# Optimization experiments

Hardware: AMD Instinct MI355X
Metric: run time of the kernel (lower is better)

Reference implementation:

```python
import jax, jax.numpy as jnp
import numpy as np
import math

B, T, D, H = 2, 2048, 1024, 16
HD = D // H  # head_dim = 64
ROPE_BASE = 10000.0


def _rope_tables(t_len, dim, base, dtype=jnp.float32):
    inv_freq = 1.0 / (base ** (jnp.arange(0, dim, 2, dtype=jnp.float32) / dim))
    t = jnp.arange(t_len, dtype=jnp.float32)
    freqs = jnp.outer(t, inv_freq)                 # [T, dim/2]
    emb = jnp.concatenate([freqs, freqs], axis=-1)  # [T, dim]
    return jnp.cos(emb).astype(dtype), jnp.sin(emb).astype(dtype)


def _rotate_half(x):
    x1, x2 = jnp.split(x, 2, axis=-1)
    return jnp.concatenate([-x2, x1], axis=-1)


def _apply_rotary(x, cos, sin):
    # x: [B,H,T,hd]; cos/sin: [T,hd] broadcast over B,H
    return x * cos[None, None, :, :] + _rotate_half(x) * sin[None, None, :, :]


def setup_inputs() -> dict:
    key = jax.random.key(0)
    ks = jax.random.split(key, 5)
    x = jax.random.normal(ks[0], (B, T, D), dtype=jnp.float32)
    Wq = jax.random.normal(ks[1], (D, D), dtype=jnp.float32) * (1.0 / math.sqrt(D))
    Wk = jax.random.normal(ks[2], (D, D), dtype=jnp.float32) * (1.0 / math.sqrt(D))
    Wv = jax.random.normal(ks[3], (D, D), dtype=jnp.float32) * (1.0 / math.sqrt(D))
    Wo = jax.random.normal(ks[4], (D, D), dtype=jnp.float32) * (1.0 / math.sqrt(D))
    # additive causal mask: 0 on/below diagonal, -inf above
    neg = jnp.finfo(jnp.float32).min
    mask = jnp.where(jnp.tril(jnp.ones((T, T), dtype=bool)), 0.0, neg).astype(jnp.float32)
    return {"x": x, "mask": mask, "Wq": Wq, "Wk": Wk, "Wv": Wv, "Wo": Wo}


def reference(x, mask, Wq, Wk, Wv, Wo):
    scale = math.sqrt(HD)
    # projections (nn.Linear: y = x @ W.T), split heads -> [B,H,T,hd]
    q = jnp.einsum('btd,ed->bte', x, Wq).reshape(B, T, H, HD).transpose(0, 2, 1, 3)
    k = jnp.einsum('btd,ed->bte', x, Wk).reshape(B, T, H, HD).transpose(0, 2, 1, 3)
    v = jnp.einsum('btd,ed->bte', x, Wv).reshape(B, T, H, HD).transpose(0, 2, 1, 3)
    cos, sin = _rope_tables(T, HD, ROPE_BASE, x.dtype)
    q = _apply_rotary(q, cos, sin)
    k = _apply_rotary(k, cos, sin)
    scores = jnp.einsum('bhqd,bhkd->bhqk', q, k) / scale   # [B,H,T,T]
    scores = scores + mask[None, None, :, :]
    attn_weights = jax.nn.softmax(scores, axis=-1)          # [B,H,T,T]
    # dropout=0.0 (eval): attn_weights_dropped == attn_weights
    out = jnp.einsum('bhqk,bhkd->bhqd', attn_weights, v)    # [B,H,T,hd]
    out = out.transpose(0, 2, 1, 3).reshape(B, T, D)
    out = jnp.einsum('btd,ed->bte', out, Wo)
    return out, attn_weights
```

## Files before the change

### kernel.cpp

```cpp
#include <hip/hip_runtime.h>
#include <math.h>

#define Tn 2048
#define Dn 1024
#define Hn 16
#define HDn 64

typedef float f32x4 __attribute__((ext_vector_type(4)));
typedef _Float16 f16x8 __attribute__((ext_vector_type(8)));
typedef _Float16 f16x4 __attribute__((ext_vector_type(4)));
typedef __fp16 fp16x2 __attribute__((ext_vector_type(2)));

__device__ __forceinline__ f32x4 mfma16(f16x8 a, f16x8 b, f32x4 c) {
  return __builtin_amdgcn_mfma_f32_16x16x32_f16(a, b, c, 0, 0, 0);
}

__device__ __forceinline__ void cvt_store4(_Float16* dst, float4 v) {
  union { _Float16 h[4]; uint2 u; } pk;
  pk.h[0] = (_Float16)v.x; pk.h[1] = (_Float16)v.y;
  pk.h[2] = (_Float16)v.z; pk.h[3] = (_Float16)v.w;
  *reinterpret_cast<uint2*>(dst) = pk.u;
}

__device__ __forceinline__ void nt_store4v(float* p, f32x4 t) {
  __builtin_nontemporal_store(t, reinterpret_cast<f32x4*>(p));
}

__device__ __forceinline__ f16x4 pk4(float a, float b, float c, float d) {
  union { fp16x2 v[2]; f16x4 h; } u;
  u.v[0] = __builtin_amdgcn_cvt_pkrtz(a, b);
  u.v[1] = __builtin_amdgcn_cvt_pkrtz(c, d);
  return u.h;
}

__device__ __forceinline__ void gld16(const _Float16* g, _Float16* l) {
  __builtin_amdgcn_global_load_lds(
      (const __attribute__((address_space(1))) uint32_t*)g,
      (__attribute__((address_space(3))) uint32_t*)l, 16, 0, 0);
}

#define SOFT_SYNC do {                                        \
    __builtin_amdgcn_sched_barrier(0);                        \
    asm volatile("s_waitcnt lgkmcnt(0)" ::: "memory");        \
    __builtin_amdgcn_s_barrier();                             \
    __builtin_amdgcn_sched_barrier(0);                        \
  } while (0)

__global__ __launch_bounds__(256) void cvt_fp16_kernel(
    const float* __restrict__ x, const float* __restrict__ wq,
    const float* __restrict__ wk, const float* __restrict__ wv,
    const float* __restrict__ wo,
    _Float16* __restrict__ xh, _Float16* __restrict__ wqh,
    _Float16* __restrict__ wkh, _Float16* __restrict__ wvh,
    _Float16* __restrict__ woh)
{
  int i = blockIdx.x * 256 + threadIdx.x;
  const float* src; _Float16* dst; int off;
  if (i < 1048576) { src = x; dst = xh; off = i; }
  else {
    int j = i - 1048576;
    int w = j >> 18; off = j & 262143;
    src = (w == 0) ? wq : (w == 1) ? wk : (w == 2) ? wv : wo;
    dst = (w == 0) ? wqh : (w == 1) ? wkh : (w == 2) ? wvh : woh;
  }
  float4 v = reinterpret_cast<const float4*>(src)[off];
  cvt_store4(dst + (size_t)off * 4, v);
}

__global__ void rope_table_kernel(float* __restrict__ cosT, float* __restrict__ sinT) {
  int i = blockIdx.x * 256 + threadIdx.x;
  if (i >= Tn * 32) return;
  int t = i >> 5, f = i & 31;
  float inv = powf(10000.0f, -(float)(2 * f) / 64.0f);
  float ang = (float)t * inv;
  float c = cosf(ang), s = sinf(ang);
  cosT[t * HDn + f] = c; cosT[t * HDn + f + 32] = c;
  sinT[t * HDn + f] = s; sinT[t * HDn + f + 32] = s;
}

__global__ __launch_bounds__(256) void proj_kernel(
    const _Float16* __restrict__ xh, const _Float16* __restrict__ wqh,
    const _Float16* __restrict__ wkh, const _Float16* __restrict__ wvh,
    const float* __restrict__ cosT, const float* __restrict__ sinT,
    _Float16* __restrict__ qh, _Float16* __restrict__ kh, _Float16* __restrict__ vh)
{
  const int w = blockIdx.z;
  const _Float16* __restrict__ W = (w == 0) ? wqh : (w == 1) ? wkh : wvh;
  _Float16* __restrict__ dst = (w == 0) ? qh : (w == 1) ? kh : vh;
  __shared__ alignas(16) _Float16 As[128 * 64];
  __shared__ alignas(16) _Float16 Bs[128 * 64];
  const int tid = threadIdx.x;
  const int lane = tid & 63, wave = tid >> 6;
  const int lrow = lane & 15, lhi = lane >> 4;
  const int wm = wave >> 1, wn = wave & 1;
  const int f = blockIdx.x, s = f >> 3;
  const int mt = (f & 7) + 8 * (s & 3);
  const int ntl = s >> 2;
  const int m0 = mt * 128, n0 = ntl * 128;
  f32x4 acc[4][4];
#pragma unroll
  for (int i = 0; i < 4; ++i)
#pragma unroll
    for (int j = 0; j < 4; ++j) acc[i][j] = f32x4{0.f, 0.f, 0.f, 0.f};

  for (int k0 = 0; k0 < Dn; k0 += 64) {
#pragma unroll
    for (int it = 0; it < 4; ++it) {
      int n = it * 256 + tid;
      int row = n >> 3, cc = n & 7;
      int csw = cc ^ (row & 7);
      _Float16* lbase = As + (size_t)(it * 256 + wave * 64) * 8;
      gld16(xh + (size_t)(m0 + row) * Dn + k0 + csw * 8, lbase);
      _Float16* lbase2 = Bs + (size_t)(it * 256 + wave * 64) * 8;
      gld16(W + (size_t)(n0 + row) * Dn + k0 + csw * 8, lbase2);
    }
    __syncthreads();
#pragma unroll
    for (int kc = 0; kc < 2; ++kc) {
      f16x8 af[4], bf[4];
#pragma unroll
      for (int i = 0; i < 4; ++i) {
        int row = wm * 64 + i * 16 + lrow;
        af[i] = *reinterpret_cast<const f16x8*>(
            As + row * 64 + (((kc * 4 + lhi) ^ (row & 7)) << 3));
      }
#pragma unroll
      for (int j = 0; j < 4; ++j) {
        int row = wn * 64 + j * 16 + lrow;
        bf[j] = *reinterpret_cast<const f16x8*>(
            Bs + row * 64 + (((kc * 4 + lhi) ^ (row & 7)) << 3));
      }
#pragma unroll
      for (int i = 0; i < 4; ++i)
#pragma unroll
        for (int j = 0; j < 4; ++j)
          acc[i][j] = mfma16(af[i], bf[j], acc[i][j]);
    }
    __syncthreads();
  }
  const bool isqk = (w < 2);
#pragma unroll
  for (int i = 0; i < 4; ++i) {
#pragma unroll
    for (int r = 0; r < 4; ++r) {
      int rowg = m0 + wm * 64 + i * 16 + lhi * 4 + r;
      int bb = rowg >> 11, t = rowg & (Tn - 1);
#pragma unroll
      for (int j = 0; j < 4; ++j) {
        int colg = n0 + wn * 64 + j * 16 + lrow;
        int hh = colg >> 6, d = colg & 63;
        float val = acc[i][j][r];
        if (isqk) {
          float partner = acc[i][j ^ 2][r];
          float rot = (j < 2) ? -partner : partner;
          val = val * cosT[t * HDn + d] + rot * sinT[t * HDn + d];
        }
        dst[(((size_t)(bb * Hn + hh)) * Tn + t) * HDn + d] = (_Float16)val;
      }
    }
  }
}

__global__ __launch_bounds__(256) void attn_kernel(
    const _Float16* __restrict__ qh, const _Float16* __restrict__ kh,
    const _Float16* __restrict__ vh, float* __restrict__ attnw,
    _Float16* __restrict__ obuf)
{
  const int f = blockIdx.x;
  const int s = f >> 3, g = s >> 5;
  const int my_bh = (f & 7) + 8 * g;
  const int c = ((s & 31) + 8 * g) & 31;
  const int b = my_bh >> 4, h = my_bh & 15;
  const size_t bh = (size_t)my_bh;
  const _Float16* __restrict__ Qp = qh + bh * Tn * HDn;
  const _Float16* __restrict__ Kp = kh + bh * Tn * HDn;
  const _Float16* __restrict__ Vp = vh + bh * Tn * HDn;
  float* __restrict__ attnp = attnw + bh * (size_t)Tn * Tn;

  __shared__ _Float16 Ks[128][72];
  __shared__ _Float16 Vt[64][136];
  __shared__ _Float16 Pt[4][16][136];

  const int tid = threadIdx.x;
  const int lane = tid & 63, wave = tid >> 6;
  const int q16 = lane & 15, lhi = lane >> 4;
  const int qp0 = c * 64;
  const int wrow = qp0 + wave * 16;
  const int qg = wrow + q16;
  const int ntiles = (c >> 1) + 1;

  f16x8 bq[2];
#pragma unroll
  for (int kc = 0; kc < 2; ++kc) {
    bq[kc] = *reinterpret_cast<const f16x8*>(
        Qp + (size_t)qg * HDn + kc * 32 + lhi * 8);
    bq[kc] = bq[kc] * (_Float16)0.18033688f;
  }

  float lsum = 0.f;
  for (int kt = 0; kt < ntiles; ++kt) {
#pragma unroll
    for (int it = 0; it < 4; ++it) {
      int idx = it * 2048 + tid * 8;
      int r = idx >> 6, cc = idx & 63;
      *reinterpret_cast<uint4*>(&Ks[r][cc]) =
          *reinterpret_cast<const uint4*>(Kp + (size_t)(kt * 128 + r) * HDn + cc);
    }
    SOFT_SYNC;
    f32x4 st[8];
#pragma unroll
    for (int nf = 0; nf < 8; ++nf) st[nf] = f32x4{0.f, 0.f, 0.f, 0.f};
#pragma unroll
    for (int kc = 0; kc < 2; ++kc) {
      f16x8 ak[8];
#pragma unroll
      for (int nf = 0; nf < 8; ++nf)
        ak[nf] = *reinterpret_cast<const f16x8*>(&Ks[nf * 16 + q16][kc * 32 + lhi * 8]);
#pragma unroll
      for (int nf = 0; nf < 8; ++nf) st[nf] = mfma16(ak[nf], bq[kc], st[nf]);
    }
    const bool diag = (kt == ntiles - 1);
#pragma unroll
    for (int nf = 0; nf < 8; ++nf) {
      int kbase = kt * 128 + nf * 16 + lhi * 4;
#pragma unroll
      for (int r = 0; r < 4; ++r) {
        float v = st[nf][r];
        if (diag && (kbase + r) > qg) v = -INFINITY;
        lsum += __builtin_amdgcn_exp2f(v);
      }
    }
    SOFT_SYNC;
  }
  lsum += __shfl_xor(lsum, 16);
  lsum += __shfl_xor(lsum, 32);
  const float lg = __builtin_amdgcn_logf(lsum);

  f32x4 oacc[4];
#pragma unroll
  for (int df = 0; df < 4; ++df) oacc[df] = f32x4{0.f, 0.f, 0.f, 0.f};

  for (int kt = 0; kt < ntiles; ++kt) {
#pragma unroll
    for (int it = 0; it < 4; ++it) {
      int idx = it * 2048 + tid * 8;
      int r = idx >> 6, cc = idx & 63;
      *reinterpret_cast<uint4*>(&Ks[r][cc]) =
          *reinterpret_cast<const uint4*>(Kp + (size_t)(kt * 128 + r) * HDn + cc);
      uint4 vv = *reinterpret_cast<const uint4*>(Vp + (size_t)(kt * 128 + r) * HDn + cc);
      const _Float16* pv = reinterpret_cast<const _Float16*>(&vv);
      int colb = ((((r >> 3) ^ (cc >> 3)) & 15) << 3) | (r & 7);
#pragma unroll
      for (int j = 0; j < 8; ++j) Vt[cc + j][colb] = pv[j];
    }
    SOFT_SYNC;
    f32x4 st[8];
#pragma unroll
    for (int nf = 0; nf < 8; ++nf) st[nf] = f32x4{0.f, 0.f, 0.f, 0.f};
#pragma unroll
    for (int kc = 0; kc < 2; ++kc) {
      f16x8 ak[8];
#pragma unroll
      for (int nf = 0; nf < 8; ++nf)
        ak[nf] = *reinterpret_cast<const f16x8*>(&Ks[nf * 16 + q16][kc * 32 + lhi * 8]);
#pragma unroll
      for (int nf = 0; nf < 8; ++nf) st[nf] = mfma16(ak[nf], bq[kc], st[nf]);
    }
    const bool diag = (kt == ntiles - 1);
#pragma unroll
    for (int nf = 0; nf < 8; ++nf) {
      int kbase = kt * 128 + nf * 16 + lhi * 4;
      float p[4];
#pragma unroll
      for (int r = 0; r < 4; ++r) {
        float v = st[nf][r];
        if (diag && (kbase + r) > qg) v = -INFINITY;
        p[r] = __builtin_amdgcn_exp2f(v - lg);
      }
      *reinterpret_cast<f16x4*>(&Pt[wave][q16][nf * 16 + lhi * 4]) =
          pk4(p[0], p[1], p[2], p[3]);
    }
#pragma unroll
    for (int kc2 = 0; kc2 < 4; ++kc2) {
      f16x8 ap = *reinterpret_cast<const f16x8*>(&Pt[wave][q16][kc2 * 32 + lhi * 8]);
      f16x8 bv[4];
#pragma unroll
      for (int df = 0; df < 4; ++df) {
        int d = df * 16 + q16;
        int colb = (((4 * kc2 + lhi) ^ ((d >> 3) & 7)) & 15) << 3;
        bv[df] = *reinterpret_cast<const f16x8*>(&Vt[d][colb]);
      }
#pragma unroll
      for (int df = 0; df < 4; ++df) oacc[df] = mfma16(ap, bv[df], oacc[df]);
    }
    {
      const int qrd = (lane >> 5);
      const int k4 = (lane & 31) * 4;
#pragma unroll
      for (int it2 = 0; it2 < 8; ++it2) {
        int qrow = it2 * 2 + qrd;
        f16x4 ph = *reinterpret_cast<const f16x4*>(&Pt[wave][qrow][k4]);
        f32x4 pf;
        pf[0] = (float)ph[0]; pf[1] = (float)ph[1];
        pf[2] = (float)ph[2]; pf[3] = (float)ph[3];
        nt_store4v(attnp + (size_t)(wrow + qrow) * Tn + kt * 128 + k4, pf);
      }
    }
    SOFT_SYNC;
  }

#pragma unroll
  for (int df = 0; df < 4; ++df)
#pragma unroll
    for (int r = 0; r < 4; ++r)
      obuf[((size_t)(b * Tn + wrow + lhi * 4 + r)) * Dn + h * HDn + df * 16 + q16] =
          (_Float16)oacc[df][r];

  int zc0 = ntiles * 128;
  if (zc0 < Tn) {
    int n4 = (Tn - zc0) >> 2;
    int total = 64 * n4;
    for (int i = tid; i < total; i += 256) {
      int r = i / n4, cc = (i - r * n4) * 4;
      f32x4 z = f32x4{0.f, 0.f, 0.f, 0.f};
      nt_store4v(attnp + (size_t)(qp0 + r) * Tn + zc0 + cc, z);
    }
  }
}

__global__ __launch_bounds__(256) void outproj_kernel(
    const _Float16* __restrict__ obuf, const _Float16* __restrict__ woh,
    float* __restrict__ out)
{
  __shared__ alignas(16) _Float16 As[128 * 64];
  __shared__ alignas(16) _Float16 Bs[128 * 64];
  const int tid = threadIdx.x;
  const int lane = tid & 63, wave = tid >> 6;
  const int lrow = lane & 15, lhi = lane >> 4;
  const int wm = wave >> 1, wn = wave & 1;
  const int f = blockIdx.x, s = f >> 3;
  const int mt = (f & 7) + 8 * (s & 3);
  const int ntl = s >> 2;
  const int m0 = mt * 128, n0 = ntl * 128;
  f32x4 acc[4][4];
#pragma unroll
  for (int i = 0; i < 4; ++i)
#pragma unroll
    for (int j = 0; j < 4; ++j) acc[i][j] = f32x4{0.f, 0.f, 0.f, 0.f};

  for (int k0 = 0; k0 < Dn; k0 += 64) {
#pragma unroll
    for (int it = 0; it < 4; ++it) {
      int n = it * 256 + tid;
      int row = n >> 3, cc = n & 7;
      int csw = cc ^ (row & 7);
      _Float16* lbase = As + (size_t)(it * 256 + wave * 64) * 8;
      gld16(obuf + (size_t)(m0 + row) * Dn + k0 + csw * 8, lbase);
      _Float16* lbase2 = Bs + (size_t)(it * 256 + wave * 64) * 8;
      gld16(woh + (size_t)(n0 + row) * Dn + k0 + csw * 8, lbase2);
    }
    __syncthreads();
#pragma unroll
    for (int kc = 0; kc < 2; ++kc) {
      f16x8 af[4], bf[4];
#pragma unroll
      for (int i = 0; i < 4; ++i) {
        int row = wm * 64 + i * 16 + lrow;
        af[i] = *reinterpret_cast<const f16x8*>(
            As + row * 64 + (((kc * 4 + lhi) ^ (row & 7)) << 3));
      }
#pragma unroll
      for (int j = 0; j < 4; ++j) {
        int row = wn * 64 + j * 16 + lrow;
        bf[j] = *reinterpret_cast<const f16x8*>(
            Bs + row * 64 + (((kc * 4 + lhi) ^ (row & 7)) << 3));
      }
#pragma unroll
      for (int i = 0; i < 4; ++i)
#pragma unroll
        for (int j = 0; j < 4; ++j)
          acc[i][j] = mfma16(af[i], bf[j], acc[i][j]);
    }
    __syncthreads();
  }
#pragma unroll
  for (int i = 0; i < 4; ++i)
#pragma unroll
    for (int j = 0; j < 4; ++j)
#pragma unroll
      for (int r = 0; r < 4; ++r) {
        int rowg = m0 + wm * 64 + i * 16 + lhi * 4 + r;
        int colg = n0 + wn * 64 + j * 16 + lrow;
        out[(size_t)rowg * Dn + colg] = acc[i][j][r];
      }
}

extern "C" void kernel_launch(void* const* d_in, const int* in_sizes, int n_in,
                              void* d_out, int out_size, void* d_ws, size_t ws_size,
                              hipStream_t stream) {
  const float* x  = (const float*)d_in[0];
  const float* Wq = (const float*)d_in[2];
  const float* Wk = (const float*)d_in[3];
  const float* Wv = (const float*)d_in[4];
  const float* Wo = (const float*)d_in[5];

  float* out   = (float*)d_out;
  float* attnw = out + (size_t)2 * Tn * Dn;

  char* ws = (char*)d_ws;
  float* cosT = (float*)ws;
  float* sinT = cosT + Tn * HDn;
  _Float16* xh   = (_Float16*)(sinT + Tn * HDn);
  _Float16* obuf = xh;
  _Float16* wqh  = xh + (size_t)2 * Tn * Dn;
  _Float16* wkh  = wqh + Dn * Dn;
  _Float16* wvh  = wkh + Dn * Dn;
  _Float16* woh  = wvh + Dn * Dn;
  _Float16* qh   = woh + Dn * Dn;
  _Float16* kh   = qh + (size_t)2 * Tn * Dn;
  _Float16* vh   = kh + (size_t)2 * Tn * Dn;

  cvt_fp16_kernel<<<dim3(8192), 256, 0, stream>>>(x, Wq, Wk, Wv, Wo,
                                                  xh, wqh, wkh, wvh, woh);
  rope_table_kernel<<<dim3(256), 256, 0, stream>>>(cosT, sinT);
  proj_kernel<<<dim3(256, 1, 3), 256, 0, stream>>>(xh, wqh, wkh, wvh,
                                                   cosT, sinT, qh, kh, vh);
  attn_kernel<<<dim3(1024), 256, 0, stream>>>(qh, kh, vh, attnw, obuf);
  outproj_kernel<<<dim3(256), 256, 0, stream>>>(obuf, woh, out);
}
```

Before: 223.4 us.

## Fuse Q, K and V projections into one block sharing the x tile

The projection kernel now computes Q, K and V together for each 128-row x tile. It loads the x tile into LDS once and keeps three weight tiles alongside it, instead of launching a separate grid slice per weight matrix. Blocks grow to 512 threads, and each wave owns 16 rows by 128 columns for all three outputs, with RoPE applied in the epilogue. This cuts redundant global reads of x and launches one-third as many blocks. The cost is more LDS fragment loads per MFMA, more accumulator registers, and a grid of only 256 large blocks.

```diff
diff --git a/kernel.cpp b/kernel.cpp
--- a/kernel.cpp
+++ b/kernel.cpp
@@ -78,81 +78,88 @@
   sinT[t * HDn + f] = s; sinT[t * HDn + f + 32] = s;
 }
 
-__global__ __launch_bounds__(256) void proj_kernel(
+__global__ __launch_bounds__(512) void proj_kernel(
     const _Float16* __restrict__ xh, const _Float16* __restrict__ wqh,
     const _Float16* __restrict__ wkh, const _Float16* __restrict__ wvh,
     const float* __restrict__ cosT, const float* __restrict__ sinT,
     _Float16* __restrict__ qh, _Float16* __restrict__ kh, _Float16* __restrict__ vh)
 {
-  const int w = blockIdx.z;
-  const _Float16* __restrict__ W = (w == 0) ? wqh : (w == 1) ? wkh : wvh;
-  _Float16* __restrict__ dst = (w == 0) ? qh : (w == 1) ? kh : vh;
   __shared__ alignas(16) _Float16 As[128 * 64];
-  __shared__ alignas(16) _Float16 Bs[128 * 64];
+  __shared__ alignas(16) _Float16 Bs[3][128 * 64];
   const int tid = threadIdx.x;
   const int lane = tid & 63, wave = tid >> 6;
   const int lrow = lane & 15, lhi = lane >> 4;
-  const int wm = wave >> 1, wn = wave & 1;
-  const int f = blockIdx.x, s = f >> 3;
-  const int mt = (f & 7) + 8 * (s & 3);
-  const int ntl = s >> 2;
+  const int f = blockIdx.x;
+  const int ntl = f & 7;
+  const int mt = f >> 3;
   const int m0 = mt * 128, n0 = ntl * 128;
-  f32x4 acc[4][4];
-#pragma unroll
-  for (int i = 0; i < 4; ++i)
-#pragma unroll
-    for (int j = 0; j < 4; ++j) acc[i][j] = f32x4{0.f, 0.f, 0.f, 0.f};
+
+  f32x4 acc[3][8];
+#pragma unroll
+  for (int w3 = 0; w3 < 3; ++w3)
+#pragma unroll
+    for (int nf = 0; nf < 8; ++nf) acc[w3][nf] = f32x4{0.f, 0.f, 0.f, 0.f};
 
   for (int k0 = 0; k0 < Dn; k0 += 64) {
 #pragma unroll
-    for (int it = 0; it < 4; ++it) {
-      int n = it * 256 + tid;
+    for (int it = 0; it < 2; ++it) {
+      int n = it * 512 + tid;
       int row = n >> 3, cc = n & 7;
       int csw = cc ^ (row & 7);
-      _Float16* lbase = As + (size_t)(it * 256 + wave * 64) * 8;
-      gld16(xh + (size_t)(m0 + row) * Dn + k0 + csw * 8, lbase);
-      _Float16* lbase2 = Bs + (size_t)(it * 256 + wave * 64) * 8;
-      gld16(W + (size_t)(n0 + row) * Dn + k0 + csw * 8, lbase2);
+      _Float16* lb = As + (size_t)(it * 512 + wave * 64) * 8;
+      gld16(xh + (size_t)(m0 + row) * Dn + k0 + csw * 8, lb);
+      {
+        _Float16* lb2 = Bs[0] + (size_t)(it * 512 + wave * 64) * 8;
+        gld16(wqh + (size_t)(n0 + row) * Dn + k0 + csw * 8, lb2);
+      }
+      {
+        _Float16* lb2 = Bs[1] + (size_t)(it * 512 + wave * 64) * 8;
+        gld16(wkh + (size_t)(n0 + row) * Dn + k0 + csw * 8, lb2);
+      }
+      {
+        _Float16* lb2 = Bs[2] + (size_t)(it * 512 + wave * 64) * 8;
+        gld16(wvh + (size_t)(n0 + row) * Dn + k0 + csw * 8, lb2);
+      }
     }
     __syncthreads();
 #pragma unroll
     for (int kc = 0; kc < 2; ++kc) {
-      f16x8 af[4], bf[4];
-#pragma unroll
-      for (int i = 0; i < 4; ++i) {
-        int row = wm * 64 + i * 16 + lrow;
-        af[i] = *reinterpret_cast<const f16x8*>(
-            As + row * 64 + (((kc * 4 + lhi) ^ (row & 7)) << 3));
-      }
-#pragma unroll
-      for (int j = 0; j < 4; ++j) {
-        int row = wn * 64 + j * 16 + lrow;
-        bf[j] = *reinterpret_cast<const f16x8*>(
-            Bs + row * 64 + (((kc * 4 + lhi) ^ (row & 7)) << 3));
-      }
-#pragma unroll
-      for (int i = 0; i < 4; ++i)
-#pragma unroll
-        for (int j = 0; j < 4; ++j)
-          acc[i][j] = mfma16(af[i], bf[j], acc[i][j]);
+      int arow = wave * 16 + lrow;
+      f16x8 af = *reinterpret_cast<const f16x8*>(
+          As + arow * 64 + (((kc * 4 + lhi) ^ (arow & 7)) << 3));
+#pragma unroll
+      for (int w3 = 0; w3 < 3; ++w3) {
+        f16x8 bf[8];
+#pragma unroll
+        for (int nf = 0; nf < 8; ++nf) {
+          int brow = nf * 16 + lrow;
+          bf[nf] = *reinterpret_cast<const f16x8*>(
+              Bs[w3] + brow * 64 + (((kc * 4 + lhi) ^ (brow & 7)) << 3));
+        }
+#pragma unroll
+        for (int nf = 0; nf < 8; ++nf)
+          acc[w3][nf] = mfma16(af, bf[nf], acc[w3][nf]);
+      }
     }
     __syncthreads();
   }
-  const bool isqk = (w < 2);
-#pragma unroll
-  for (int i = 0; i < 4; ++i) {
-#pragma unroll
-    for (int r = 0; r < 4; ++r) {
-      int rowg = m0 + wm * 64 + i * 16 + lhi * 4 + r;
-      int bb = rowg >> 11, t = rowg & (Tn - 1);
-#pragma unroll
-      for (int j = 0; j < 4; ++j) {
-        int colg = n0 + wn * 64 + j * 16 + lrow;
+
+#pragma unroll
+  for (int w3 = 0; w3 < 3; ++w3) {
+    _Float16* __restrict__ dst = (w3 == 0) ? qh : (w3 == 1) ? kh : vh;
+    const bool isqk = (w3 < 2);
+#pragma unroll
+    for (int nf = 0; nf < 8; ++nf) {
+#pragma unroll
+      for (int r = 0; r < 4; ++r) {
+        int rowg = m0 + wave * 16 + lhi * 4 + r;
+        int bb = rowg >> 11, t = rowg & (Tn - 1);
+        int colg = n0 + nf * 16 + lrow;
         int hh = colg >> 6, d = colg & 63;
-        float val = acc[i][j][r];
+        float val = acc[w3][nf][r];
         if (isqk) {
-          float partner = acc[i][j ^ 2][r];
-          float rot = (j < 2) ? -partner : partner;
+          float partner = acc[w3][nf ^ 2][r];
+          float rot = ((nf & 2) == 0) ? -partner : partner;
           val = val * cosT[t * HDn + d] + rot * sinT[t * HDn + d];
         }
         dst[(((size_t)(bb * Hn + hh)) * Tn + t) * HDn + d] = (_Float16)val;
@@ -423,8 +430,8 @@
   cvt_fp16_kernel<<<dim3(8192), 256, 0, stream>>>(x, Wq, Wk, Wv, Wo,
                                                   xh, wqh, wkh, wvh, woh);
   rope_table_kernel<<<dim3(256), 256, 0, stream>>>(cosT, sinT);
-  proj_kernel<<<dim3(256, 1, 3), 256, 0, stream>>>(xh, wqh, wkh, wvh,
-                                                   cosT, sinT, qh, kh, vh);
+  proj_kernel<<<dim3(256), 512, 0, stream>>>(xh, wqh, wkh, wvh,
+                                             cosT, sinT, qh, kh, vh);
   attn_kernel<<<dim3(1024), 256, 0, stream>>>(qh, kh, vh, attnw, obuf);
   outproj_kernel<<<dim3(256), 256, 0, stream>>>(obuf, woh, out);
 }
```

After: 216.1 us (median of 3 runs). 3.2% less time.
